# Performance work log

Measured on AMD Instinct MI355X. Metric: run time of the kernel, lower is better.

## Reference

```python
import jax, jax.numpy as jnp
import numpy as np

# PEPS grid configuration (matches init_kwargs)
X, Y = 4, 4            # xnodes, ynodes
D = 6                  # bond_dim
P = 2                  # features_in (physical dim)
F = 10                 # features_out (forced by result.view([10]))
CX, CY = X // 2, Y // 2  # center node carries the output leg
BATCH = 2048


def node_labels(i, j):
    # bond labels after the physical index is contracted away; axis order: up, left, down, right, out
    labs = []
    if i > 0: labs.append(f'v{i-1}_{j}')   # up bond (shared with row i-1)
    if j > 0: labs.append(f'h{i}_{j-1}')   # left bond (shared with col j-1)
    if i < X - 1: labs.append(f'v{i}_{j}') # down bond
    if j < Y - 1: labs.append(f'h{i}_{j}') # right bond
    if (i, j) == (CX, CY): labs.append('o')  # output leg on center node
    return labs


def node_shape(i, j):
    shp = [P]  # physical axis first (input_nodes[i][j][0] ^ peps_nodes[i][j][0])
    shp += [D] * (int(i > 0) + int(j > 0) + int(i < X - 1) + int(j < Y - 1))
    if (i, j) == (CX, CY): shp.append(F)
    return tuple(shp)


def setup_inputs() -> dict:
    key = jax.random.key(0)
    keys = jax.random.split(key, X * Y + 1)
    inp = {"x": jax.random.normal(keys[0], (BATCH, X, Y, P), dtype=jnp.float32)}
    k = 1
    for i in range(X):
        for j in range(Y):
            # simple_peps uniform init with std=0.01
            inp[f"w{i}{j}"] = jax.random.uniform(keys[k], node_shape(i, j), dtype=jnp.float32, minval=-0.01, maxval=0.01)
            k += 1
    return inp


def _td(a, alabs, b, blabs):
    """Label-tracked tensordot over all shared bond labels."""
    shared = [l for l in alabs if l in blabs]
    ai = [alabs.index(l) for l in shared]
    bi = [blabs.index(l) for l in shared]
    out = jnp.tensordot(a, b, axes=(ai, bi))
    labs = [l for l in alabs if l not in shared] + [l for l in blabs if l not in shared]
    return out, labs


def _contract_sample(xs, ws):
    # xs: [X, Y, P] one sample; ws: list-of-lists of node tensors
    # 1) contract each input vector into its PEPS node over the physical axis,
    #    then L2-normalize each contracted node (as in func())
    nodes = []
    for i in range(X):
        row = []
        for j in range(Y):
            t = jnp.tensordot(xs[i, j], ws[i][j], axes=(0, 0))
            t = t / jnp.linalg.norm(t)
            row.append(t)
        nodes.append(row)
    # 2) exact contraction of the 2D network, row-by-row boundary sweep
    cur, labs = nodes[0][0], node_labels(0, 0)
    for j in range(1, Y):
        cur, labs = _td(cur, labs, nodes[0][j], node_labels(0, j))
    for i in range(1, X):
        for j in range(Y):
            cur, labs = _td(cur, labs, nodes[i][j], node_labels(i, j))
    out = cur.reshape(F)  # result.view([10])
    return out / jnp.linalg.norm(out)


def reference(x, w00, w01, w02, w03, w10, w11, w12, w13,
              w20, w21, w22, w23, w30, w31, w32, w33):
    ws = [[w00, w01, w02, w03],
          [w10, w11, w12, w13],
          [w20, w21, w22, w23],
          [w30, w31, w32, w33]]
    return jax.vmap(lambda s: _contract_sample(s, ws))(x)  # [B, F]
```

## Files before the change

kernel.cpp:

```cpp
#include <hip/hip_runtime.h>
#include <math.h>

#define NTHREADS 256

struct PW {
    const float* w[16];
    int perp[16];
};

__global__ __launch_bounds__(NTHREADS) void gram64(PW pw, float* __restrict__ g) {
    const int n = blockIdx.x >> 2, sl = blockIdx.x & 3;
    const float* __restrict__ W = pw.w[n];
    const int m = pw.perp[n];
    float s00 = 0.f, s01 = 0.f, s11 = 0.f;
    for (int e = (sl * NTHREADS + threadIdx.x) * 4; e < m; e += NTHREADS * 16) {
        const float4 a = *reinterpret_cast<const float4*>(W + e);
        const float4 b = *reinterpret_cast<const float4*>(W + m + e);
        s00 += a.x * a.x + a.y * a.y + a.z * a.z + a.w * a.w;
        s01 += a.x * b.x + a.y * b.y + a.z * b.z + a.w * b.w;
        s11 += b.x * b.x + b.y * b.y + b.z * b.z + b.w * b.w;
    }
    for (int off = 32; off > 0; off >>= 1) {
        s00 += __shfl_down(s00, off, 64);
        s01 += __shfl_down(s01, off, 64);
        s11 += __shfl_down(s11, off, 64);
    }
    __shared__ float red[4][3];
    const int lane = threadIdx.x & 63, wv = threadIdx.x >> 6;
    if (lane == 0) { red[wv][0] = s00; red[wv][1] = s01; red[wv][2] = s11; }
    __syncthreads();
    if (threadIdx.x == 0) {
        float t0 = 0.f, t1 = 0.f, t2 = 0.f;
        for (int i = 0; i < 4; i++) { t0 += red[i][0]; t1 += red[i][1]; t2 += red[i][2]; }
        g[n * 12 + sl * 3 + 0] = t0; g[n * 12 + sl * 3 + 1] = t1; g[n * 12 + sl * 3 + 2] = t2;
    }
}

constexpr int SA = 0, SB = 1296, SC = 2592, SP = 3888;
constexpr int W0A = 4104, W2A = 4140, W20A = 4356, W31A = 4572, W3A = 4788;
constexpr int ARENA = 5004;

template<int D0, int D1, int D2, int D3, int S0, int S1, int S2, int S3, int DST>
__device__ __forceinline__ void stg_pm(float* __restrict__ lds, const float* __restrict__ W,
                                       float a0, float b0, float a1, float b1, int tid) {
    constexpr int TOT = D0 * D1 * D2 * D3;
    for (int e = tid; e < 2 * TOT; e += NTHREADS) {
        const int s = (e >= TOT);
        const int d = e - s * TOT;
        int r = d;
        const int i3 = r % D3; r /= D3;
        const int i2 = r % D2; r /= D2;
        const int i1 = r % D1;
        const int i0 = r / D1;
        const int src = i0 * S0 + i1 * S1 + i2 * S2 + i3 * S3;
        const float al = s ? a1 : a0, be = s ? b1 : b0;
        lds[s * ARENA + DST + d] = al * W[src] + be * W[TOT + src];
    }
}

#define PK_FMA(ACC, AV, BV) { (ACC).x += (AV) * (BV).x; (ACC).y += (AV) * (BV).y; }

template<int M, int N, int K, int TM, int TN, int AOFF, int BOFF>
__device__ __forceinline__ void mm_acc(const float* __restrict__ lds, int tid,
                                       float2 (&acc)[TM][TN / 2]) {
    constexpr int WM = M / TM, WN = N / TN, PER_S = WM * WN, TOT = 2 * PER_S;
    static_assert(TOT <= NTHREADS, "tile overflow");
    if (tid >= TOT) return;
    const int s = (tid >= PER_S);
    const int r = tid - s * PER_S;
    const int mt = r / WN, nt = r - mt * WN;
    const float* __restrict__ Ab = lds + s * ARENA + AOFF + mt * TM;
    const float* __restrict__ Bb = lds + s * ARENA + BOFF + nt * TN;
#pragma unroll
    for (int i = 0; i < TM; i++)
#pragma unroll
        for (int j = 0; j < TN / 2; j++) { acc[i][j].x = 0.f; acc[i][j].y = 0.f; }
#pragma unroll 6
    for (int k = 0; k < K; ++k) {
        float a[TM]; float2 b[TN / 2];
        if constexpr (TM == 4) {
            const float4 v = *reinterpret_cast<const float4*>(Ab + k * M);
            a[0] = v.x; a[1] = v.y; a[2] = v.z; a[3] = v.w;
        } else {
            const float2 v = *reinterpret_cast<const float2*>(Ab + k * M);
            a[0] = v.x; a[1] = v.y;
        }
        if constexpr (TN == 4) {
            const float4 v = *reinterpret_cast<const float4*>(Bb + k * N);
            b[0].x = v.x; b[0].y = v.y; b[1].x = v.z; b[1].y = v.w;
        } else {
            b[0] = *reinterpret_cast<const float2*>(Bb + k * N);
        }
#pragma unroll
        for (int i = 0; i < TM; i++)
#pragma unroll
            for (int j = 0; j < TN / 2; j++) PK_FMA(acc[i][j], a[i], b[j]);
    }
}

template<int M, int N, int K, int TM, int TN, int AOFF, int PL>
__device__ __forceinline__ void mm_accGB(const float* __restrict__ lds,
                                         const float* __restrict__ W,
                                         float a0, float b0, float a1, float b1,
                                         int tid, float2 (&acc)[TM][TN / 2]) {
    constexpr int WM = M / TM, WN = N / TN, PER_S = WM * WN, TOT = 2 * PER_S;
    static_assert(TOT <= NTHREADS, "tile overflow");
    if (tid >= TOT) return;
    const int s = (tid >= PER_S);
    const int r = tid - s * PER_S;
    const int mt = r / WN, nt = r - mt * WN;
    const float al = s ? a1 : a0, be = s ? b1 : b0;
    const float* __restrict__ Ab = lds + s * ARENA + AOFF + mt * TM;
    const float* __restrict__ Bb = W + nt * TN;
#pragma unroll
    for (int i = 0; i < TM; i++)
#pragma unroll
        for (int j = 0; j < TN / 2; j++) { acc[i][j].x = 0.f; acc[i][j].y = 0.f; }
#pragma unroll 6
    for (int k = 0; k < K; ++k) {
        float a[TM]; float2 b[TN / 2];
        if constexpr (TM == 4) {
            const float4 v = *reinterpret_cast<const float4*>(Ab + k * M);
            a[0] = v.x; a[1] = v.y; a[2] = v.z; a[3] = v.w;
        } else {
            const float2 v = *reinterpret_cast<const float2*>(Ab + k * M);
            a[0] = v.x; a[1] = v.y;
        }
        if constexpr (TN == 4) {
            const float4 u0 = *reinterpret_cast<const float4*>(Bb + k * N);
            const float4 u1 = *reinterpret_cast<const float4*>(Bb + PL + k * N);
            b[0].x = al * u0.x + be * u1.x; b[0].y = al * u0.y + be * u1.y;
            b[1].x = al * u0.z + be * u1.z; b[1].y = al * u0.w + be * u1.w;
        } else {
            const float2 u0 = *reinterpret_cast<const float2*>(Bb + k * N);
            const float2 u1 = *reinterpret_cast<const float2*>(Bb + PL + k * N);
            b[0].x = al * u0.x + be * u1.x; b[0].y = al * u0.y + be * u1.y;
        }
#pragma unroll
        for (int i = 0; i < TM; i++)
#pragma unroll
            for (int j = 0; j < TN / 2; j++) PK_FMA(acc[i][j], a[i], b[j]);
    }
}

template<int M, int N, int K, int TM, int TN, int BOFF, int PL>
__device__ __forceinline__ void mm_accGA(const float* __restrict__ lds,
                                         const float* __restrict__ W,
                                         float a0, float b0, float a1, float b1,
                                         int tid, float2 (&acc)[TM][TN / 2]) {
    constexpr int WM = M / TM, WN = N / TN, PER_S = WM * WN, TOT = 2 * PER_S;
    static_assert(TOT <= NTHREADS, "tile overflow");
    if (tid >= TOT) return;
    const int s = (tid >= PER_S);
    const int r = tid - s * PER_S;
    const int mt = r / WN, nt = r - mt * WN;
    const float al = s ? a1 : a0, be = s ? b1 : b0;
    const float* __restrict__ Ab = W + mt * TM;
    const float* __restrict__ Bb = lds + s * ARENA + BOFF + nt * TN;
#pragma unroll
    for (int i = 0; i < TM; i++)
#pragma unroll
        for (int j = 0; j < TN / 2; j++) { acc[i][j].x = 0.f; acc[i][j].y = 0.f; }
#pragma unroll 6
    for (int k = 0; k < K; ++k) {
        float a[TM]; float2 b[TN / 2];
        if constexpr (TM == 4) {
            const float4 u0 = *reinterpret_cast<const float4*>(Ab + k * M);
            const float4 u1 = *reinterpret_cast<const float4*>(Ab + PL + k * M);
            a[0] = al * u0.x + be * u1.x; a[1] = al * u0.y + be * u1.y;
            a[2] = al * u0.z + be * u1.z; a[3] = al * u0.w + be * u1.w;
        } else {
            const float2 u0 = *reinterpret_cast<const float2*>(Ab + k * M);
            const float2 u1 = *reinterpret_cast<const float2*>(Ab + PL + k * M);
            a[0] = al * u0.x + be * u1.x; a[1] = al * u0.y + be * u1.y;
        }
        if constexpr (TN == 4) {
            const float4 v = *reinterpret_cast<const float4*>(Bb + k * N);
            b[0].x = v.x; b[0].y = v.y; b[1].x = v.z; b[1].y = v.w;
        } else {
            b[0] = *reinterpret_cast<const float2*>(Bb + k * N);
        }
#pragma unroll
        for (int i = 0; i < TM; i++)
#pragma unroll
            for (int j = 0; j < TN / 2; j++) PK_FMA(acc[i][j], a[i], b[j]);
    }
}

template<int TM, int TNH>
__device__ __forceinline__ float accv(const float2 (&acc)[TM][TNH], int i, int j) {
    return (j & 1) ? acc[i][j >> 1].y : acc[i][j >> 1].x;
}

template<int M, int N, int TM, int TN,
         int NM2, int OSM1, int OSM2, int NN2, int OSN1, int OSN2, int OOFF>
__device__ __forceinline__ void mm_wr(float* __restrict__ lds, int tid,
                                      const float2 (&acc)[TM][TN / 2]) {
    constexpr int WM = M / TM, WN = N / TN, PER_S = WM * WN, TOT = 2 * PER_S;
    if (tid >= TOT) return;
    const int s = (tid >= PER_S);
    const int r = tid - s * PER_S;
    const int mt = r / WN, nt = r - mt * WN;
    float* __restrict__ Ob = lds + s * ARENA + OOFF;
    constexpr bool NCONT = (TN == 4) && (OSN2 == 1) && ((NN2 >= N) || (OSN1 == NN2));
    constexpr bool MCONT = (TM == 4) && (OSM2 == 1) && ((NM2 >= M) || (OSM1 == NM2));
    if constexpr (NCONT) {
        const int nb = nt * TN;
#pragma unroll
        for (int i = 0; i < TM; i++) {
            const int m = mt * TM + i;
            int m1, m2;
            if constexpr (NM2 >= M) { m1 = 0; m2 = m; }
            else                    { m1 = m / NM2; m2 = m - m1 * NM2; }
            float4 v; v.x = acc[i][0].x; v.y = acc[i][0].y; v.z = acc[i][1].x; v.w = acc[i][1].y;
            *reinterpret_cast<float4*>(Ob + m1 * OSM1 + m2 * OSM2 + nb) = v;
        }
    } else if constexpr (MCONT) {
        const int mb = mt * TM;
#pragma unroll
        for (int j = 0; j < TN; j++) {
            const int n = nt * TN + j;
            int n1, n2;
            if constexpr (NN2 >= N) { n1 = 0; n2 = n; }
            else                    { n1 = n / NN2; n2 = n - n1 * NN2; }
            float4 v;
            v.x = accv(acc, 0, j); v.y = accv(acc, 1, j);
            v.z = accv(acc, 2, j); v.w = accv(acc, 3, j);
            *reinterpret_cast<float4*>(Ob + n1 * OSN1 + n2 * OSN2 + mb) = v;
        }
    } else {
#pragma unroll
        for (int i = 0; i < TM; i++) {
            const int m = mt * TM + i;
            int m1, m2;
            if constexpr (NM2 >= M) { m1 = 0; m2 = m; }
            else                    { m1 = m / NM2; m2 = m - m1 * NM2; }
#pragma unroll
            for (int j = 0; j < TN; j++) {
                const int n = nt * TN + j;
                int n1, n2;
                if constexpr (NN2 >= N) { n1 = 0; n2 = n; }
                else                    { n1 = n / NN2; n2 = n - n1 * NN2; }
                Ob[m1 * OSM1 + m2 * OSM2 + n1 * OSN1 + n2 * OSN2] = accv(acc, i, j);
            }
        }
    }
}

template<int M, int N, int K, int TM, int TN,
         int NM2, int OSM1, int OSM2, int NN2, int OSN1, int OSN2,
         int AOFF, int BOFF, int OOFF>
__device__ __forceinline__ void mmd(float* __restrict__ lds, int tid) {
    float2 acc[TM][TN / 2];
    mm_acc<M, N, K, TM, TN, AOFF, BOFF>(lds, tid, acc);
    mm_wr<M, N, TM, TN, NM2, OSM1, OSM2, NN2, OSN1, OSN2, OOFF>(lds, tid, acc);
}

template<int M, int N, int K, int TM, int TN,
         int NM2, int OSM1, int OSM2, int NN2, int OSN1, int OSN2,
         int AOFF, int PL, int OOFF>
__device__ __forceinline__ void mmdGB(float* __restrict__ lds, const float* __restrict__ W,
                                      float a0, float b0, float a1, float b1, int tid) {
    float2 acc[TM][TN / 2];
    mm_accGB<M, N, K, TM, TN, AOFF, PL>(lds, W, a0, b0, a1, b1, tid, acc);
    mm_wr<M, N, TM, TN, NM2, OSM1, OSM2, NN2, OSN1, OSN2, OOFF>(lds, tid, acc);
}

template<int M, int N, int K, int TM, int TN,
         int NM2, int OSM1, int OSM2, int NN2, int OSN1, int OSN2,
         int BOFF, int PL, int OOFF>
__device__ __forceinline__ void mmdGA(float* __restrict__ lds, const float* __restrict__ W,
                                      float a0, float b0, float a1, float b1, int tid) {
    float2 acc[TM][TN / 2];
    mm_accGA<M, N, K, TM, TN, BOFF, PL>(lds, W, a0, b0, a1, b1, tid, acc);
    mm_wr<M, N, TM, TN, NM2, OSM1, OSM2, NN2, OSN1, OSN2, OOFF>(lds, tid, acc);
}

__global__ __launch_bounds__(NTHREADS, 4) void peps_main(const float* __restrict__ x, PW pw,
                                                         const float* __restrict__ gram,
                                                         float* __restrict__ out) {
    __shared__ float lds[2 * ARENA];
    __shared__ float cfa[2][16], cfb[2][16];
    __shared__ float red[4][10];

    const int tid = threadIdx.x;
    const int s0 = blockIdx.x * 2;

    if (tid < 32) {
        const int sl = tid >> 4, n = tid & 15;
        const float a = x[(s0 + sl) * 32 + n * 2 + 0];
        const float b = x[(s0 + sl) * 32 + n * 2 + 1];
        float g0 = 0.f, g1 = 0.f, g2 = 0.f;
#pragma unroll
        for (int q = 0; q < 4; q++) {
            g0 += gram[n * 12 + q * 3 + 0];
            g1 += gram[n * 12 + q * 3 + 1];
            g2 += gram[n * 12 + q * 3 + 2];
        }
        const float inv = 1.f / sqrtf(a * a * g0 + 2.f * a * b * g1 + b * b * g2);
        cfa[sl][n] = a * inv; cfb[sl][n] = b * inv;
    }
    __syncthreads();

#define CF(WI) cfa[0][WI], cfb[0][WI], cfa[1][WI], cfb[1][WI]

    stg_pm<6, 6, 6, 6, 216, 1, 36, 6, SC>(lds, pw.w[6], CF(6), tid);
    stg_pm<1, 1, 6, 6, 0, 0, 1, 6, W0A>(lds, pw.w[0], CF(0), tid);
    stg_pm<1, 6, 6, 6, 0, 1, 36, 6, W2A>(lds, pw.w[2], CF(2), tid);
    stg_pm<1, 6, 6, 6, 0, 6, 36, 1, W20A>(lds, pw.w[8], CF(8), tid);
    stg_pm<1, 6, 6, 6, 0, 6, 36, 1, W31A>(lds, pw.w[13], CF(13), tid);
    stg_pm<1, 6, 6, 6, 0, 1, 36, 6, W3A>(lds, pw.w[14], CF(14), tid);
    __syncthreads();

    mmdGB<6, 36, 6, 2, 4, 6, 0, 36, 36, 0, 1, W0A, 216, SP>(lds, pw.w[1], CF(1), tid);
    __syncthreads();

    mmdGB<36, 36, 6, 4, 4, 6, 216, 6, 6, 1, 36, SP, 216, SA>(lds, pw.w[4], CF(4), tid);
    __syncthreads();

    mmdGB<36, 36, 36, 4, 4, 6, 216, 6, 6, 1, 36, SA, 1296, SB>(lds, pw.w[5], CF(5), tid);
    mmdGB<36, 6, 6, 4, 2, 36, 0, 1, 6, 0, 36, W2A, 36, SP>(lds, pw.w[3], CF(3), tid);
    __syncthreads();

    mmdGB<36, 36, 6, 4, 4, 6, 6, 216, 6, 36, 1, SP, 216, SA>(lds, pw.w[7], CF(7), tid);
    __syncthreads();

    {
        float2 a6[4][2];
        mm_acc<36, 36, 36, 4, 4, SC, SA>(lds, tid, a6);
        __syncthreads();
        mm_wr<36, 36, 4, 4, 6, 36, 6, 6, 216, 1, SA>(lds, tid, a6);
    }
    __syncthreads();

    {
        float2 a7[4][2];
        mm_acc<36, 36, 36, 4, 4, SB, SA>(lds, tid, a7);
        stg_pm<6, 6, 6, 6, 36, 6, 216, 1, SC>(lds, pw.w[9], CF(9), tid);
        mmdGA<6, 36, 6, 2, 4, 6, 0, 36, 36, 0, 1, W20A, 36, SP>(lds, pw.w[12], CF(12), tid);
        __syncthreads();
        mm_wr<36, 36, 4, 4, 6, 216, 36, 6, 6, 1, SB>(lds, tid, a7);
    }
    __syncthreads();

    mmd<36, 36, 6, 4, 4, 6, 6, 216, 6, 36, 1, SP, W31A, SA>(lds, tid);
    stg_pm<1, 6, 6, 6, 0, 1, 36, 6, W2A>(lds, pw.w[11], CF(11), tid);
    __syncthreads();

    {
        float2 a10[4][2];
        mm_acc<36, 36, 36, 4, 4, SA, SC>(lds, tid, a10);
        __syncthreads();
        mm_wr<36, 36, 4, 4, 6, 216, 6, 6, 36, 1, SA>(lds, tid, a10);
    }
    __syncthreads();

    mmd<36, 36, 36, 4, 4, 6, 6, 216, 6, 36, 1, SB, SA, SC>(lds, tid);
    mmdGB<36, 6, 6, 4, 2, 36, 0, 1, 6, 0, 36, W2A, 36, SP>(lds, pw.w[15], CF(15), tid);
    __syncthreads();

    mmd<36, 36, 6, 4, 4, 6, 216, 1, 6, 6, 36, SP, W3A, SB>(lds, tid);
    __syncthreads();

    mmd<36, 36, 36, 4, 4, 6, 216, 36, 6, 6, 1, SC, SB, SA>(lds, tid);
    __syncthreads();

    {
        const int half = tid >> 7;
        const int t = tid & 127;
        const float aC = cfa[half][10], bC = cfb[half][10];
        const float* __restrict__ w0 = pw.w[10];
        const float* __restrict__ w1 = w0 + 12960;
        float p[10];
#pragma unroll
        for (int o = 0; o < 10; o++) p[o] = 0.f;
        for (int f = t; f < 324; f += 128) {
            const float4 E = *reinterpret_cast<const float4*>(lds + half * ARENA + SA + 4 * f);
            const float ev[4] = {E.x, E.y, E.z, E.w};
#pragma unroll
            for (int u = 0; u < 4; u++) {
                const int e = 4 * f + u;
                const float* __restrict__ q0 = w0 + e * 10;
                const float* __restrict__ q1 = w1 + e * 10;
#pragma unroll
                for (int o = 0; o < 10; o++)
                    p[o] += ev[u] * (aC * q0[o] + bC * q1[o]);
            }
        }
#pragma unroll
        for (int o = 0; o < 10; o++)
            for (int off = 32; off > 0; off >>= 1)
                p[o] += __shfl_down(p[o], off, 64);
        const int lane = tid & 63, wv = tid >> 6;
        if (lane == 0) {
#pragma unroll
            for (int o = 0; o < 10; o++) red[wv][o] = p[o];
        }
        __syncthreads();
        if (tid < 2) {
            float r[10];
            float ss = 0.f;
#pragma unroll
            for (int o = 0; o < 10; o++) {
                r[o] = red[2 * tid][o] + red[2 * tid + 1][o];
                ss += r[o] * r[o];
            }
            const float inv = 1.f / sqrtf(ss);
#pragma unroll
            for (int o = 0; o < 10; o++) out[(s0 + tid) * 10 + o] = r[o] * inv;
        }
    }
#undef CF
}

extern "C" void kernel_launch(void* const* d_in, const int* in_sizes, int n_in,
                              void* d_out, int out_size, void* d_ws, size_t ws_size,
                              hipStream_t stream) {
    PW pw;
    for (int k = 0; k < 16; k++) {
        pw.w[k] = (const float*)d_in[1 + k];
        pw.perp[k] = in_sizes[1 + k] / 2;
    }
    float* gram = (float*)d_ws;
    gram64<<<64, NTHREADS, 0, stream>>>(pw, gram);

    const float* x = (const float*)d_in[0];
    const int B = out_size / 10;
    peps_main<<<B / 2, NTHREADS, 0, stream>>>(x, pw, gram, (float*)d_out);
}
```

Baseline: 138.9 us.

## Fuse gram-norm precomputation into main kernel, removing separate launch

Removes the separate gram64 kernel launch and has every block of peps_main recompute the per-node Gram sums (||w0||², <w0,w1>, ||w1||²) into shared memory, with the work split across its four wavefronts. This eliminates one kernel launch and the dependency on the gram workspace. In exchange, each of the 1024 blocks now redundantly reads all node weights (roughly 30K floats) before starting, which adds global or L2 traffic and a serial prologue per block, and the per-wave work is unbalanced.

```diff
diff --git a/kernel.cpp b/kernel.cpp
--- a/kernel.cpp
+++ b/kernel.cpp
@@ -7,34 +7,6 @@
     const float* w[16];
     int perp[16];
 };
-
-__global__ __launch_bounds__(NTHREADS) void gram64(PW pw, float* __restrict__ g) {
-    const int n = blockIdx.x >> 2, sl = blockIdx.x & 3;
-    const float* __restrict__ W = pw.w[n];
-    const int m = pw.perp[n];
-    float s00 = 0.f, s01 = 0.f, s11 = 0.f;
-    for (int e = (sl * NTHREADS + threadIdx.x) * 4; e < m; e += NTHREADS * 16) {
-        const float4 a = *reinterpret_cast<const float4*>(W + e);
-        const float4 b = *reinterpret_cast<const float4*>(W + m + e);
-        s00 += a.x * a.x + a.y * a.y + a.z * a.z + a.w * a.w;
-        s01 += a.x * b.x + a.y * b.y + a.z * b.z + a.w * b.w;
-        s11 += b.x * b.x + b.y * b.y + b.z * b.z + b.w * b.w;
-    }
-    for (int off = 32; off > 0; off >>= 1) {
-        s00 += __shfl_down(s00, off, 64);
-        s01 += __shfl_down(s01, off, 64);
-        s11 += __shfl_down(s11, off, 64);
-    }
-    __shared__ float red[4][3];
-    const int lane = threadIdx.x & 63, wv = threadIdx.x >> 6;
-    if (lane == 0) { red[wv][0] = s00; red[wv][1] = s01; red[wv][2] = s11; }
-    __syncthreads();
-    if (threadIdx.x == 0) {
-        float t0 = 0.f, t1 = 0.f, t2 = 0.f;
-        for (int i = 0; i < 4; i++) { t0 += red[i][0]; t1 += red[i][1]; t2 += red[i][2]; }
-        g[n * 12 + sl * 3 + 0] = t0; g[n * 12 + sl * 3 + 1] = t1; g[n * 12 + sl * 3 + 2] = t2;
-    }
-}
 
 constexpr int SA = 0, SB = 1296, SC = 2592, SP = 3888;
 constexpr int W0A = 4104, W2A = 4140, W20A = 4356, W31A = 4572, W3A = 4788;
@@ -58,6 +30,30 @@
     }
 }
 
+__device__ __forceinline__ void gram_node(const PW& pw, int node, int start, int count,
+                                          int lane, int wv, float* __restrict__ gpart) {
+    const float* __restrict__ W = pw.w[node];
+    const int m = pw.perp[node];
+    float s00 = 0.f, s01 = 0.f, s11 = 0.f;
+    for (int q = start / 4 + lane; q < (start + count) / 4; q += 64) {
+        const float4 a = *reinterpret_cast<const float4*>(W + 4 * q);
+        const float4 b = *reinterpret_cast<const float4*>(W + m + 4 * q);
+        s00 += a.x * a.x + a.y * a.y + a.z * a.z + a.w * a.w;
+        s01 += a.x * b.x + a.y * b.y + a.z * b.z + a.w * b.w;
+        s11 += b.x * b.x + b.y * b.y + b.z * b.z + b.w * b.w;
+    }
+    for (int off = 32; off > 0; off >>= 1) {
+        s00 += __shfl_down(s00, off, 64);
+        s01 += __shfl_down(s01, off, 64);
+        s11 += __shfl_down(s11, off, 64);
+    }
+    if (lane == 0) {
+        gpart[(node * 4 + wv) * 3 + 0] = s00;
+        gpart[(node * 4 + wv) * 3 + 1] = s01;
+        gpart[(node * 4 + wv) * 3 + 2] = s11;
+    }
+}
+
 #define PK_FMA(ACC, AV, BV) { (ACC).x += (AV) * (BV).x; (ACC).y += (AV) * (BV).y; }
 
 template<int M, int N, int K, int TM, int TN, int AOFF, int BOFF>
@@ -277,7 +273,6 @@
 }
 
 __global__ __launch_bounds__(NTHREADS, 4) void peps_main(const float* __restrict__ x, PW pw,
-                                                         const float* __restrict__ gram,
                                                          float* __restrict__ out) {
     __shared__ float lds[2 * ARENA];
     __shared__ float cfa[2][16], cfb[2][16];
@@ -285,6 +280,34 @@
 
     const int tid = threadIdx.x;
     const int s0 = blockIdx.x * 2;
+    const int lane = tid & 63, wv = tid >> 6;
+
+    if (tid < 192) lds[tid] = 0.f;
+    __syncthreads();
+    {
+        gram_node(pw, 10, wv * 3240, 3240, lane, wv, lds);
+        if (wv == 0) {
+            gram_node(pw, 5, 0, 1296, lane, wv, lds);
+            gram_node(pw, 0, 0, 36, lane, wv, lds);
+        } else if (wv == 1) {
+            gram_node(pw, 6, 0, 1296, lane, wv, lds);
+            gram_node(pw, 3, 0, 36, lane, wv, lds);
+        } else if (wv == 2) {
+            gram_node(pw, 9, 0, 1296, lane, wv, lds);
+            gram_node(pw, 12, 0, 36, lane, wv, lds);
+            gram_node(pw, 14, 0, 216, lane, wv, lds);
+        } else {
+            gram_node(pw, 1, 0, 216, lane, wv, lds);
+            gram_node(pw, 2, 0, 216, lane, wv, lds);
+            gram_node(pw, 4, 0, 216, lane, wv, lds);
+            gram_node(pw, 7, 0, 216, lane, wv, lds);
+            gram_node(pw, 8, 0, 216, lane, wv, lds);
+            gram_node(pw, 11, 0, 216, lane, wv, lds);
+            gram_node(pw, 13, 0, 216, lane, wv, lds);
+            gram_node(pw, 15, 0, 36, lane, wv, lds);
+        }
+    }
+    __syncthreads();
 
     if (tid < 32) {
         const int sl = tid >> 4, n = tid & 15;
@@ -293,9 +316,9 @@
         float g0 = 0.f, g1 = 0.f, g2 = 0.f;
 #pragma unroll
         for (int q = 0; q < 4; q++) {
-            g0 += gram[n * 12 + q * 3 + 0];
-            g1 += gram[n * 12 + q * 3 + 1];
-            g2 += gram[n * 12 + q * 3 + 2];
+            g0 += lds[(n * 4 + q) * 3 + 0];
+            g1 += lds[(n * 4 + q) * 3 + 1];
+            g2 += lds[(n * 4 + q) * 3 + 2];
         }
         const float inv = 1.f / sqrtf(a * a * g0 + 2.f * a * b * g1 + b * b * g2);
         cfa[sl][n] = a * inv; cfb[sl][n] = b * inv;
@@ -391,7 +414,6 @@
         for (int o = 0; o < 10; o++)
             for (int off = 32; off > 0; off >>= 1)
                 p[o] += __shfl_down(p[o], off, 64);
-        const int lane = tid & 63, wv = tid >> 6;
         if (lane == 0) {
 #pragma unroll
             for (int o = 0; o < 10; o++) red[wv][o] = p[o];
@@ -421,10 +443,7 @@
         pw.w[k] = (const float*)d_in[1 + k];
         pw.perp[k] = in_sizes[1 + k] / 2;
     }
-    float* gram = (float*)d_ws;
-    gram64<<<64, NTHREADS, 0, stream>>>(pw, gram);
-
     const float* x = (const float*)d_in[0];
     const int B = out_size / 10;
-    peps_main<<<B / 2, NTHREADS, 0, stream>>>(x, pw, gram, (float*)d_out);
-}
+    peps_main<<<B / 2, NTHREADS, 0, stream>>>(x, pw, (float*)d_out);
+}
```

New measurement: 144.4 us. 4.0% more time.
